# Kernel tuning notes

Hardware: AMD Instinct MI355X
Metric: run time of the kernel (lower is better)

## Reference

```python
import jax, jax.numpy as jnp
import numpy as np

FT = 0.2  # clip floor (init arg ft)

def _norm_mat(m):
    # matrix / (count of nonzeros along last dim + 1e-30)
    deg = jnp.sum(m != 0, axis=-1, keepdims=True).astype(m.dtype)
    return m / (deg + 1e-30)

def _l2n(x):
    return x / (jnp.linalg.norm(x, axis=-1, keepdims=True) + 1e-30)

def setup_inputs():
    B, L, D, H, O = 2, 2048, 64, 64, 128
    N = 2 * L
    ks = jax.random.split(jax.random.key(0), 30)
    u = lambda i, s: jax.random.uniform(ks[i], s, jnp.float32)
    g = lambda i, s: jax.random.normal(ks[i], s, jnp.float32) * 0.05
    inp = {}
    inp['word_outputs_0'] = g(0, (B, L, D))
    inp['word_outputs_1'] = g(1, (B, L, D))
    inp['node_hidden'] = g(2, (B, D))
    inp['op_embedding'] = g(3, (B, O, D))
    inp['word_exist_sequence'] = (u(4, (B, N)) < 0.8).astype(jnp.float32)
    inp['word_exist_matrix'] = (u(5, (B, N, N)) < 0.8).astype(jnp.float32)
    inp['word_operator'] = (u(6, (B, N, O)) < 0.02).astype(jnp.float32)
    inp['word_word'] = (u(7, (B, N, N)) < 0.01).astype(jnp.float32)
    inp['depend_0'] = (u(8, (B, L, L)) < 0.05).astype(jnp.float32)
    inp['depend_1'] = (u(9, (B, L, L)) < 0.05).astype(jnp.float32)
    inp['goal_word'] = u(10, (B, N))
    names = [('Wg', (D, H)), ('bg', (H,)), ('Wwk', (D, H)), ('bwk', (H,)),
             ('Wws', (D, H)), ('bws', (H,)), ('Wo', (D, D)), ('bo', (D,)),
             ('Wupd', (3 * H, D)), ('bupd', (D,)), ('Wf', (3 * H + D, D)), ('bf', (D,)),
             ('Wf2', (2 * D, D)), ('bf2', (D,)), ('Wout', (D, D)), ('bout', (D,))]
    for i, (nm, s) in enumerate(names):
        inp[nm] = g(11 + i, s)
    return inp

def _forward(w0, w1, nh, opE, wes, wem, wop, ww, d0, d1, gw,
             Wg, bg, Wwk, bwk, Wws, bws, Wo, bo, Wupd, bupd, Wf, bf, Wf2, bf2, Wout, bout):
    all_w = jnp.concatenate([w0, w1], axis=1)                      # [B,N,D]
    goal_trans = (nh @ Wg + bg)[:, None, :]                        # [B,1,H] (broadcast = expand)
    word_g = _l2n(goal_trans * gw[..., None])                      # [B,N,H]
    word_w_k = _l2n(jnp.matmul(_norm_mat(ww * wem), all_w @ Wwk + bwk))
    ws0 = jnp.matmul(_norm_mat(d0), w0 @ Wws + bws)
    ws1 = jnp.matmul(_norm_mat(d1), w1 @ Wws + bws)
    word_w_s = _l2n(jnp.concatenate([ws0, ws1], axis=1))           # [B,N,H]
    neigh = jnp.concatenate([word_g, word_w_k, word_w_s], axis=-1)  # [B,N,3H]
    forget = jax.nn.sigmoid(jnp.concatenate([all_w, word_g, word_w_k, word_w_s], axis=-1) @ Wf + bf)
    word_updated = jnp.maximum(forget, FT) * all_w + (1.0 - forget) * jax.nn.relu(neigh @ Wupd + bupd)
    adj_op = _norm_mat(jnp.swapaxes(wes[..., None] * wop, 1, 2))   # [B,O,N]
    word_op = jnp.matmul(adj_op, word_updated @ Wo + bo)           # [B,O,D]
    forget2 = jax.nn.sigmoid(jnp.concatenate([opE, word_op], axis=-1) @ Wf2 + bf2)
    op_out = jnp.maximum(forget2, FT) * opE + (1.0 - forget2) * jax.nn.relu(word_op @ Wout + bout)
    # original returns (split(word_updated), op_embedding); concat along node axis here
    return jnp.concatenate([word_updated, op_out], axis=1)         # [B,N+O,D]

def reference(word_outputs_0, word_outputs_1, node_hidden, op_embedding,
              word_exist_sequence, word_exist_matrix, word_operator, word_word,
              depend_0, depend_1, goal_word,
              Wg, bg, Wwk, bwk, Wws, bws, Wo, bo, Wupd, bupd, Wf, bf, Wf2, bf2, Wout, bout):
    return _forward(word_outputs_0, word_outputs_1, node_hidden, op_embedding,
                    word_exist_sequence, word_exist_matrix, word_operator, word_word,
                    depend_0, depend_1, goal_word,
                    Wg, bg, Wwk, bwk, Wws, bws, Wo, bo, Wupd, bupd, Wf, bf, Wf2, bf2, Wout, bout)
```

## Files before the change

kernel.cpp:

```cpp
#include <hip/hip_runtime.h>
#include <cstdint>

typedef unsigned short u16;
typedef unsigned long long u64;

__device__ __forceinline__ u16 f2b(float f){
  union { float f; uint32_t i; } v; v.f = f;
  uint32_t r = v.i + 0x7FFFu + ((v.i >> 16) & 1u);
  return (u16)(r >> 16);
}
__device__ __forceinline__ float b2f(u16 u){
  union { uint32_t i; float f; } v; v.i = ((uint32_t)u) << 16; return v.f;
}
__device__ __forceinline__ float sigmoidf(float x){ return 1.0f / (1.0f + __expf(-x)); }

__global__ void k_pre(const float* __restrict__ nh, const float* __restrict__ Wg,
                      const float* __restrict__ bg, float* __restrict__ ghat){
  int b = threadIdx.x >> 6, h = threadIdx.x & 63;
  float g = bg[h];
  for (int d = 0; d < 64; ++d) g += nh[b*64 + d] * Wg[d*64 + h];
  float ss = g * g;
  #pragma unroll
  for (int o = 32; o > 0; o >>= 1) ss += __shfl_xor(ss, o, 64);
  ghat[b*64 + h] = g / (sqrtf(ss) + 1e-30f);
}

__global__ __launch_bounds__(256) void k_xform(
    const float* __restrict__ w0, const float* __restrict__ w1,
    const float* __restrict__ Wwk, const float* __restrict__ bwk,
    const float* __restrict__ Wws, const float* __restrict__ bws,
    float* __restrict__ Xk, float* __restrict__ Xs){
  __shared__ float sWk[4096], sWs[4096];
  int tid = threadIdx.x;
  for (int i = tid; i < 1024; i += 256){
    ((float4*)sWk)[i] = ((const float4*)Wwk)[i];
    ((float4*)sWs)[i] = ((const float4*)Wws)[i];
  }
  __syncthreads();
  int lane = tid & 63, wave = tid >> 6;
  float bk = bwk[lane], bs = bws[lane];
  float aw[4];
  #pragma unroll
  for (int t = 0; t < 4; ++t){
    int row = blockIdx.x*4 + wave + t*2048;
    int b = row >> 12, n = row & 4095;
    aw[t] = (n < 2048) ? w0[((size_t)(b*2048 + n))*64 + lane]
                       : w1[((size_t)(b*2048 + n - 2048))*64 + lane];
  }
  #pragma unroll
  for (int t = 0; t < 4; ++t){
    int row = blockIdx.x*4 + wave + t*2048;
    float xk = bk, xs = bs;
    #pragma unroll 8
    for (int d = 0; d < 64; ++d){
      float a = __shfl(aw[t], d, 64);
      xk += a * sWk[d*64 + lane];
      xs += a * sWs[d*64 + lane];
    }
    Xk[(size_t)row*64 + lane] = xk;
    Xs[(size_t)row*64 + lane] = xs;
  }
}

__global__ __launch_bounds__(256) void k_bits_all(
    const float* __restrict__ ww, const float* __restrict__ wem,
    const float* __restrict__ d0, const float* __restrict__ d1,
    u64* __restrict__ bitBig, u64* __restrict__ bitD0, u64* __restrict__ bitD1){
  int wid = blockIdx.x*4 + (threadIdx.x >> 6);
  int lane = threadIdx.x & 63;
  const float *A, *B; u64* dst;
  if (wid < 32768){
    A = ww + (size_t)wid*1024; B = wem + (size_t)wid*1024; dst = bitBig + (size_t)wid*16;
  } else if (wid < 40960){
    size_t c = wid - 32768; A = d0 + c*1024; B = A; dst = bitD0 + c*16;
  } else {
    size_t c = wid - 40960; A = d1 + c*1024; B = A; dst = bitD1 + c*16;
  }
  const float4* ap = (const float4*)A + lane;
  const float4* bp = (const float4*)B + lane;
  float4 a0 = ap[0], a1 = ap[64], a2 = ap[128], a3 = ap[192];
  float4 b0 = bp[0], b1 = bp[64], b2 = bp[128], b3 = bp[192];
  u64 myw = 0;
#define B4(i, va, vb) { \
  u64 m0 = __ballot((va.x != 0.f) && (vb.x != 0.f)); \
  u64 m1 = __ballot((va.y != 0.f) && (vb.y != 0.f)); \
  u64 m2 = __ballot((va.z != 0.f) && (vb.z != 0.f)); \
  u64 m3 = __ballot((va.w != 0.f) && (vb.w != 0.f)); \
  if (lane == (i)*4 + 0) myw = m0; \
  if (lane == (i)*4 + 1) myw = m1; \
  if (lane == (i)*4 + 2) myw = m2; \
  if (lane == (i)*4 + 3) myw = m3; }
  B4(0, a0, b0) B4(1, a1, b1) B4(2, a2, b2) B4(3, a3, b3)
#undef B4
  if (lane < 16) dst[lane] = myw;
}

__global__ __launch_bounds__(64) void k_bitsop(
    const float* __restrict__ wes, const float* __restrict__ wop, u64* __restrict__ bitOp){
  int lane = threadIdx.x;
  int ng = blockIdx.x;
  float2 v = ((const float2*)(wop + (size_t)ng*128))[lane];
  float e = wes[ng];
  u64 m0 = __ballot((e != 0.f) && (v.x != 0.f));
  u64 m1 = __ballot((e != 0.f) && (v.y != 0.f));
  if (lane == 0) bitOp[(size_t)ng*2]     = m0;
  if (lane == 1) bitOp[(size_t)ng*2 + 1] = m1;
}

__global__ __launch_bounds__(256) void k_gath_all(
    const u64* __restrict__ bitBig, const u64* __restrict__ bitD0, const u64* __restrict__ bitD1,
    const float* __restrict__ Xk, const float* __restrict__ Xs,
    u16* __restrict__ wwkn, u16* __restrict__ wwsn){
  __shared__ int q[4][256];
  int lane = threadIdx.x & 63, wave = threadIdx.x >> 6;
  int wid = blockIdx.x*4 + wave;
  const u64* bits; const float* Xb; u16* op; int WPR;
  if (wid < 8192){
    WPR = 64; bits = bitBig + (size_t)wid*64;
    int b = wid >> 12;
    Xb = Xk + (size_t)b*4096*64 + lane;
    op = wwkn + (size_t)wid*64;
  } else if (wid < 12288){
    int lr = wid - 8192; WPR = 32; bits = bitD0 + (size_t)lr*32;
    int b = lr >> 11, r = lr & 2047;
    Xb = Xs + (size_t)b*4096*64 + lane;
    op = wwsn + ((size_t)b*4096 + r)*64;
  } else {
    int lr = wid - 12288; WPR = 32; bits = bitD1 + (size_t)lr*32;
    int b = lr >> 11, r = lr & 2047;
    Xb = Xs + ((size_t)b*4096 + 2048)*64 + lane;
    op = wwsn + ((size_t)b*4096 + 2048 + r)*64;
  }
  u64 word = (lane < WPR) ? bits[lane] : 0ULL;
  int c = __popcll(word);
  int pre = c;
  #pragma unroll
  for (int off = 1; off < 64; off <<= 1){
    int t = __shfl_up(pre, off, 64);
    if (lane >= off) pre += t;
  }
  int total = __shfl(pre, 63, 64);
  int base = pre - c;
  int colhi = (lane >> 2) * 256 + (lane & 3);
  u64 m = word;
  while (m){
    int p = __builtin_ctzll(m); m &= m - 1;
    q[wave][base++] = colhi + p*4;
  }
  __syncthreads();
  float acc = 0.f;
  int i = 0;
  for (; i + 8 <= total; i += 8){
    int4 c0 = *(const int4*)&q[wave][i];
    int4 c1 = *(const int4*)&q[wave][i + 4];
    float v0 = Xb[(size_t)c0.x*64], v1 = Xb[(size_t)c0.y*64];
    float v2 = Xb[(size_t)c0.z*64], v3 = Xb[(size_t)c0.w*64];
    float v4 = Xb[(size_t)c1.x*64], v5 = Xb[(size_t)c1.y*64];
    float v6 = Xb[(size_t)c1.z*64], v7 = Xb[(size_t)c1.w*64];
    acc += ((v0 + v1) + (v2 + v3)) + ((v4 + v5) + (v6 + v7));
  }
  for (; i < total; ++i) acc += Xb[(size_t)q[wave][i]*64];
  float ss = acc * acc;
  #pragma unroll
  for (int o = 32; o > 0; o >>= 1) ss += __shfl_xor(ss, o, 64);
  op[lane] = f2b(acc / (sqrtf(ss) + 1e-30f));
}

__global__ __launch_bounds__(256, 2) void k_update(
    const float* __restrict__ w0, const float* __restrict__ w1,
    const float* __restrict__ gw, const float* __restrict__ ghat,
    const u16* __restrict__ wwkn, const u16* __restrict__ wwsn,
    const float* __restrict__ Wf, const float* __restrict__ bf,
    const float* __restrict__ Wupd, const float* __restrict__ bupd,
    const float* __restrict__ Wo, const float* __restrict__ bo,
    float* __restrict__ out, float* __restrict__ WUo){
  __shared__ uint32_t pWf[8192];
  __shared__ uint32_t pWu[6144];
  __shared__ uint32_t pWo[2048];
  __shared__ float xsh[4][256];
  int tid = threadIdx.x;
  for (int i = tid; i < 8192; i += 256){
    int k2 = i >> 6, ln = i & 63;
    pWf[i] = (uint32_t)f2b(Wf[(2*k2)*64 + ln]) | ((uint32_t)f2b(Wf[(2*k2+1)*64 + ln]) << 16);
  }
  for (int i = tid; i < 6144; i += 256){
    int k2 = i >> 6, ln = i & 63;
    pWu[i] = (uint32_t)f2b(Wupd[(2*k2)*64 + ln]) | ((uint32_t)f2b(Wupd[(2*k2+1)*64 + ln]) << 16);
  }
  for (int i = tid; i < 2048; i += 256){
    int k2 = i >> 6, ln = i & 63;
    pWo[i] = (uint32_t)f2b(Wo[(2*k2)*64 + ln]) | ((uint32_t)f2b(Wo[(2*k2+1)*64 + ln]) << 16);
  }
  __syncthreads();
  int lane = tid & 63, wave = tid >> 6;
  float bff = bf[lane], bup = bupd[lane], boo = bo[lane];
  float aw[4], wgv[4], wk[4], wsv[4];
  #pragma unroll
  for (int t = 0; t < 4; ++t){
    int row = blockIdx.x*4 + wave + t*2048;
    int b = row >> 12, n = row & 4095;
    aw[t] = (n < 2048) ? w0[((size_t)(b*2048 + n))*64 + lane]
                       : w1[((size_t)(b*2048 + n - 2048))*64 + lane];
    float gvv = gw[b*4096 + n];
    wgv[t] = (gvv != 0.f) ? ghat[b*64 + lane] : 0.f;
    wk[t]  = b2f(wwkn[(size_t)row*64 + lane]);
    wsv[t] = b2f(wwsn[(size_t)row*64 + lane]);
  }
  #pragma unroll
  for (int t = 0; t < 4; ++t){
    int row = blockIdx.x*4 + wave + t*2048;
    int b = row >> 12, n = row & 4095;
    xsh[wave][lane] = aw[t]; xsh[wave][64 + lane] = wgv[t];
    xsh[wave][128 + lane] = wk[t]; xsh[wave][192 + lane] = wsv[t];
    float f = bff, u = bup;
    #pragma unroll 8
    for (int k2 = 0; k2 < 32; ++k2){
      float2 xv = *(const float2*)&xsh[wave][2*k2];
      uint32_t wf = pWf[k2*64 + lane];
      f += xv.x * b2f((u16)wf) + xv.y * b2f((u16)(wf >> 16));
    }
    #pragma unroll 8
    for (int k2 = 32; k2 < 128; ++k2){
      float2 xv = *(const float2*)&xsh[wave][2*k2];
      uint32_t wf = pWf[k2*64 + lane];
      uint32_t wu = pWu[(k2 - 32)*64 + lane];
      f += xv.x * b2f((u16)wf) + xv.y * b2f((u16)(wf >> 16));
      u += xv.x * b2f((u16)wu) + xv.y * b2f((u16)(wu >> 16));
    }
    f = sigmoidf(f);
    u = fmaxf(u, 0.f);
    float wu = fmaxf(f, 0.2f) * aw[t] + (1.f - f) * u;
    out[((size_t)b*4224 + n)*64 + lane] = wu;
    float o = boo;
    #pragma unroll 8
    for (int k2 = 0; k2 < 32; ++k2){
      uint32_t wo2 = pWo[k2*64 + lane];
      o += __shfl(wu, 2*k2, 64) * b2f((u16)wo2) + __shfl(wu, 2*k2 + 1, 64) * b2f((u16)(wo2 >> 16));
    }
    WUo[(size_t)row*64 + lane] = o;
  }
}

__global__ __launch_bounds__(256) void k_opagg(
    const u64* __restrict__ bitOp, const float* __restrict__ WUo,
    float* __restrict__ wordop){
  __shared__ int q[4][96];
  __shared__ float sacc[4][64];
  __shared__ int scnt[4];
  int tid = threadIdx.x, lane = tid & 63, wave = tid >> 6;
  int rowIdx = blockIdx.x;
  int b = rowIdx >> 7, o = rowIdx & 127;
  int wrd = o & 1, bit = o >> 1;
  const u64* bp = bitOp + (size_t)b*8192 + (size_t)wave*2048 + wrd;
  u64 lt = (1ULL << lane) - 1ULL;
  u64 vv[16];
  #pragma unroll
  for (int it = 0; it < 16; ++it) vv[it] = bp[(size_t)(it*64 + lane)*2];
  int cnt = 0;
  #pragma unroll
  for (int it = 0; it < 16; ++it){
    bool nz = (vv[it] >> bit) & 1ULL;
    u64 m = __ballot(nz);
    if (nz) q[wave][cnt + (int)__popcll(m & lt)] = wave*1024 + it*64 + lane;
    cnt += (int)__popcll(m);
  }
  const float* Xb = WUo + (size_t)b*4096*64 + lane;
  float acc = 0.f;
  int i = 0;
  for (; i + 8 <= cnt; i += 8){
    int4 c0 = *(const int4*)&q[wave][i];
    int4 c1 = *(const int4*)&q[wave][i + 4];
    float v0 = Xb[(size_t)c0.x*64], v1 = Xb[(size_t)c0.y*64];
    float v2 = Xb[(size_t)c0.z*64], v3 = Xb[(size_t)c0.w*64];
    float v4 = Xb[(size_t)c1.x*64], v5 = Xb[(size_t)c1.y*64];
    float v6 = Xb[(size_t)c1.z*64], v7 = Xb[(size_t)c1.w*64];
    acc += ((v0 + v1) + (v2 + v3)) + ((v4 + v5) + (v6 + v7));
  }
  for (; i < cnt; ++i) acc += Xb[(size_t)q[wave][i]*64];
  sacc[wave][lane] = acc;
  if (lane == 0) scnt[wave] = cnt;
  __syncthreads();
  if (wave == 0){
    float t = sacc[0][lane] + sacc[1][lane] + sacc[2][lane] + sacc[3][lane];
    float deg = (float)(scnt[0] + scnt[1] + scnt[2] + scnt[3]);
    wordop[(size_t)rowIdx*64 + lane] = t / (deg + 1e-30f);
  }
}

__global__ __launch_bounds__(256) void k_opout(
    const float* __restrict__ opE, const float* __restrict__ wordop,
    const float* __restrict__ Wf2, const float* __restrict__ bf2,
    const float* __restrict__ Wout, const float* __restrict__ bout,
    float* __restrict__ out){
  __shared__ float sW2[8192];
  __shared__ float sWo[4096];
  __shared__ float xsh[4][128];
  int tid = threadIdx.x;
  for (int i = tid; i < 2048; i += 256) ((float4*)sW2)[i] = ((const float4*)Wf2)[i];
  for (int i = tid; i < 1024; i += 256) ((float4*)sWo)[i] = ((const float4*)Wout)[i];
  __syncthreads();
  int lane = tid & 63, wave = tid >> 6;
  int row = blockIdx.x*4 + wave;
  int b = row >> 7, o = row & 127;
  float e  = opE[(size_t)row*64 + lane];
  float wo = wordop[(size_t)row*64 + lane];
  xsh[wave][lane] = e; xsh[wave][64 + lane] = wo;
  float f = bf2[lane], u = bout[lane];
  #pragma unroll 8
  for (int k = 0; k < 128; ++k) f += xsh[wave][k] * sW2[k*64 + lane];
  #pragma unroll 8
  for (int d = 0; d < 64; ++d)  u += xsh[wave][64 + d] * sWo[d*64 + lane];
  f = sigmoidf(f);
  u = fmaxf(u, 0.f);
  float res = fmaxf(f, 0.2f) * e + (1.f - f) * u;
  out[((size_t)b*4224 + 4096 + o)*64 + lane] = res;
}

extern "C" void kernel_launch(void* const* d_in, const int* in_sizes, int n_in,
                              void* d_out, int out_size, void* d_ws, size_t ws_size,
                              hipStream_t stream){
  const float* w0   = (const float*)d_in[0];
  const float* w1   = (const float*)d_in[1];
  const float* nh   = (const float*)d_in[2];
  const float* opE  = (const float*)d_in[3];
  const float* wes  = (const float*)d_in[4];
  const float* wem  = (const float*)d_in[5];
  const float* wop  = (const float*)d_in[6];
  const float* ww   = (const float*)d_in[7];
  const float* d0   = (const float*)d_in[8];
  const float* d1   = (const float*)d_in[9];
  const float* gw   = (const float*)d_in[10];
  const float* Wg   = (const float*)d_in[11];
  const float* bg   = (const float*)d_in[12];
  const float* Wwk  = (const float*)d_in[13];
  const float* bwk  = (const float*)d_in[14];
  const float* Wws  = (const float*)d_in[15];
  const float* bws  = (const float*)d_in[16];
  const float* Wo   = (const float*)d_in[17];
  const float* bo   = (const float*)d_in[18];
  const float* Wupd = (const float*)d_in[19];
  const float* bupd = (const float*)d_in[20];
  const float* Wf   = (const float*)d_in[21];
  const float* bf   = (const float*)d_in[22];
  const float* Wf2  = (const float*)d_in[23];
  const float* bf2  = (const float*)d_in[24];
  const float* Wout = (const float*)d_in[25];
  const float* bout = (const float*)d_in[26];

  float* ws   = (float*)d_ws;
  float* ghat = ws;
  float* Xk   = ws + 128;
  float* Xs   = ws + 524416;
  float* wopm = ws + 1048704;
  u64*  bitBig= (u64*)(ws + 1065088);
  u64*  bitD0 = (u64*)(ws + 2113664);
  u64*  bitD1 = (u64*)(ws + 2375808);
  u64*  bitOp = (u64*)(ws + 2637952);
  u16*  wwkn  = (u16*)(ws + 2670720);
  u16*  wwsn  = (u16*)(ws + 2932864);
  float* WUo  = Xs;
  float* out  = (float*)d_out;

  k_pre<<<1, 128, 0, stream>>>(nh, Wg, bg, ghat);
  k_xform<<<512, 256, 0, stream>>>(w0, w1, Wwk, bwk, Wws, bws, Xk, Xs);
  k_bits_all<<<12288, 256, 0, stream>>>(ww, wem, d0, d1, bitBig, bitD0, bitD1);
  k_bitsop<<<8192, 64, 0, stream>>>(wes, wop, bitOp);
  k_gath_all<<<4096, 256, 0, stream>>>(bitBig, bitD0, bitD1, Xk, Xs, wwkn, wwsn);
  k_update<<<512, 256, 0, stream>>>(w0, w1, gw, ghat, wwkn, wwsn, Wf, bf, Wupd, bupd, Wo, bo, out, WUo);
  k_opagg<<<256, 256, 0, stream>>>(bitOp, WUo, wopm);
  k_opout<<<64, 256, 0, stream>>>(opE, wopm, Wf2, bf2, Wout, bout, out);
}
```

Before: 456.7 us.

## Stage bitmask and gather loads through direct global-to-LDS loads

Switches k_bits_all to load its float rows straight into LDS with global_load_lds before the ballot, and switches k_gath_all's neighbour-row gather to batches of 16 direct-to-LDS loads followed by LDS reads. It also removes the __syncthreads after the per-wave queue build. The aim is more memory-level parallelism and fewer VGPR round trips on the bandwidth-bound bit extraction and sparse gather. The cost is extra LDS traffic and a waitcnt-based sync, and correctness depends on the global-to-LDS builtin's lane/offset semantics and on waitcnt also covering the LDS writes.

```diff
diff --git a/kernel.cpp b/kernel.cpp
--- a/kernel.cpp
+++ b/kernel.cpp
@@ -13,6 +13,16 @@
   union { uint32_t i; float f; } v; v.i = ((uint32_t)u) << 16; return v.f;
 }
 __device__ __forceinline__ float sigmoidf(float x){ return 1.0f / (1.0f + __expf(-x)); }
+
+__device__ __forceinline__ void gl_lds16(const void* g, void* l){
+  __builtin_amdgcn_global_load_lds((const __attribute__((address_space(1))) void*)g,
+                                   (__attribute__((address_space(3))) void*)l, 16, 0, 0);
+}
+__device__ __forceinline__ void gl_lds4(const void* g, void* l){
+  __builtin_amdgcn_global_load_lds((const __attribute__((address_space(1))) void*)g,
+                                   (__attribute__((address_space(3))) void*)l, 4, 0, 0);
+}
+#define WAIT_VM0() __builtin_amdgcn_s_waitcnt(0x0F70)
 
 __global__ void k_pre(const float* __restrict__ nh, const float* __restrict__ Wg,
                       const float* __restrict__ bg, float* __restrict__ ghat){
@@ -66,20 +76,33 @@
     const float* __restrict__ ww, const float* __restrict__ wem,
     const float* __restrict__ d0, const float* __restrict__ d1,
     u64* __restrict__ bitBig, u64* __restrict__ bitD0, u64* __restrict__ bitD1){
-  int wid = blockIdx.x*4 + (threadIdx.x >> 6);
-  int lane = threadIdx.x & 63;
-  const float *A, *B; u64* dst;
+  __shared__ float lA[4][1024];
+  __shared__ float lB[4][1024];
+  int wave = threadIdx.x >> 6, lane = threadIdx.x & 63;
+  int wid = blockIdx.x*4 + wave;
+  const float *A, *B; u64* dst; bool two;
   if (wid < 32768){
-    A = ww + (size_t)wid*1024; B = wem + (size_t)wid*1024; dst = bitBig + (size_t)wid*16;
+    A = ww + (size_t)wid*1024; B = wem + (size_t)wid*1024;
+    dst = bitBig + (size_t)wid*16; two = true;
   } else if (wid < 40960){
-    size_t c = wid - 32768; A = d0 + c*1024; B = A; dst = bitD0 + c*16;
+    size_t c = wid - 32768; A = d0 + c*1024; B = A; dst = bitD0 + c*16; two = false;
   } else {
-    size_t c = wid - 40960; A = d1 + c*1024; B = A; dst = bitD1 + c*16;
-  }
-  const float4* ap = (const float4*)A + lane;
-  const float4* bp = (const float4*)B + lane;
-  float4 a0 = ap[0], a1 = ap[64], a2 = ap[128], a3 = ap[192];
-  float4 b0 = bp[0], b1 = bp[64], b2 = bp[128], b3 = bp[192];
+    size_t c = wid - 40960; A = d1 + c*1024; B = A; dst = bitD1 + c*16; two = false;
+  }
+  #pragma unroll
+  for (int i = 0; i < 4; ++i)
+    gl_lds16(A + i*256 + lane*4, &lA[wave][i*256]);
+  if (two){
+    #pragma unroll
+    for (int i = 0; i < 4; ++i)
+      gl_lds16(B + i*256 + lane*4, &lB[wave][i*256]);
+  }
+  WAIT_VM0();
+  const float4* a4 = (const float4*)lA[wave];
+  const float4* b4 = (const float4*)lB[wave];
+  float4 a0 = a4[lane], a1 = a4[64 + lane], a2 = a4[128 + lane], a3 = a4[192 + lane];
+  float4 b0 = two ? b4[lane] : a0, b1 = two ? b4[64 + lane] : a1;
+  float4 b2 = two ? b4[128 + lane] : a2, b3 = two ? b4[192 + lane] : a3;
   u64 myw = 0;
 #define B4(i, va, vb) { \
   u64 m0 = __ballot((va.x != 0.f) && (vb.x != 0.f)); \
@@ -112,23 +135,24 @@
     const float* __restrict__ Xk, const float* __restrict__ Xs,
     u16* __restrict__ wwkn, u16* __restrict__ wwsn){
   __shared__ int q[4][256];
+  __shared__ float rows[4][16][64];
   int lane = threadIdx.x & 63, wave = threadIdx.x >> 6;
   int wid = blockIdx.x*4 + wave;
-  const u64* bits; const float* Xb; u16* op; int WPR;
+  const u64* bits; const float* XbBase; u16* op; int WPR;
   if (wid < 8192){
     WPR = 64; bits = bitBig + (size_t)wid*64;
     int b = wid >> 12;
-    Xb = Xk + (size_t)b*4096*64 + lane;
+    XbBase = Xk + (size_t)b*4096*64;
     op = wwkn + (size_t)wid*64;
   } else if (wid < 12288){
     int lr = wid - 8192; WPR = 32; bits = bitD0 + (size_t)lr*32;
     int b = lr >> 11, r = lr & 2047;
-    Xb = Xs + (size_t)b*4096*64 + lane;
+    XbBase = Xs + (size_t)b*4096*64;
     op = wwsn + ((size_t)b*4096 + r)*64;
   } else {
     int lr = wid - 12288; WPR = 32; bits = bitD1 + (size_t)lr*32;
     int b = lr >> 11, r = lr & 2047;
-    Xb = Xs + ((size_t)b*4096 + 2048)*64 + lane;
+    XbBase = Xs + ((size_t)b*4096 + 2048)*64;
     op = wwsn + ((size_t)b*4096 + 2048 + r)*64;
   }
   u64 word = (lane < WPR) ? bits[lane] : 0ULL;
@@ -147,19 +171,41 @@
     int p = __builtin_ctzll(m); m &= m - 1;
     q[wave][base++] = colhi + p*4;
   }
-  __syncthreads();
   float acc = 0.f;
   int i = 0;
-  for (; i + 8 <= total; i += 8){
+  for (; i + 16 <= total; i += 16){
     int4 c0 = *(const int4*)&q[wave][i];
     int4 c1 = *(const int4*)&q[wave][i + 4];
-    float v0 = Xb[(size_t)c0.x*64], v1 = Xb[(size_t)c0.y*64];
-    float v2 = Xb[(size_t)c0.z*64], v3 = Xb[(size_t)c0.w*64];
-    float v4 = Xb[(size_t)c1.x*64], v5 = Xb[(size_t)c1.y*64];
-    float v6 = Xb[(size_t)c1.z*64], v7 = Xb[(size_t)c1.w*64];
-    acc += ((v0 + v1) + (v2 + v3)) + ((v4 + v5) + (v6 + v7));
-  }
-  for (; i < total; ++i) acc += Xb[(size_t)q[wave][i]*64];
+    int4 c2 = *(const int4*)&q[wave][i + 8];
+    int4 c3 = *(const int4*)&q[wave][i + 12];
+    gl_lds4(XbBase + (size_t)c0.x*64 + lane, &rows[wave][ 0][0]);
+    gl_lds4(XbBase + (size_t)c0.y*64 + lane, &rows[wave][ 1][0]);
+    gl_lds4(XbBase + (size_t)c0.z*64 + lane, &rows[wave][ 2][0]);
+    gl_lds4(XbBase + (size_t)c0.w*64 + lane, &rows[wave][ 3][0]);
+    gl_lds4(XbBase + (size_t)c1.x*64 + lane, &rows[wave][ 4][0]);
+    gl_lds4(XbBase + (size_t)c1.y*64 + lane, &rows[wave][ 5][0]);
+    gl_lds4(XbBase + (size_t)c1.z*64 + lane, &rows[wave][ 6][0]);
+    gl_lds4(XbBase + (size_t)c1.w*64 + lane, &rows[wave][ 7][0]);
+    gl_lds4(XbBase + (size_t)c2.x*64 + lane, &rows[wave][ 8][0]);
+    gl_lds4(XbBase + (size_t)c2.y*64 + lane, &rows[wave][ 9][0]);
+    gl_lds4(XbBase + (size_t)c2.z*64 + lane, &rows[wave][10][0]);
+    gl_lds4(XbBase + (size_t)c2.w*64 + lane, &rows[wave][11][0]);
+    gl_lds4(XbBase + (size_t)c3.x*64 + lane, &rows[wave][12][0]);
+    gl_lds4(XbBase + (size_t)c3.y*64 + lane, &rows[wave][13][0]);
+    gl_lds4(XbBase + (size_t)c3.z*64 + lane, &rows[wave][14][0]);
+    gl_lds4(XbBase + (size_t)c3.w*64 + lane, &rows[wave][15][0]);
+    WAIT_VM0();
+    float s0 = 0.f, s1 = 0.f, s2 = 0.f, s3 = 0.f;
+    #pragma unroll
+    for (int r = 0; r < 4; ++r){
+      s0 += rows[wave][r][lane];
+      s1 += rows[wave][4 + r][lane];
+      s2 += rows[wave][8 + r][lane];
+      s3 += rows[wave][12 + r][lane];
+    }
+    acc += (s0 + s1) + (s2 + s3);
+  }
+  for (; i < total; ++i) acc += XbBase[(size_t)q[wave][i]*64 + lane];
   float ss = acc * acc;
   #pragma unroll
   for (int o = 32; o > 0; o >>= 1) ss += __shfl_xor(ss, o, 64);
```

New measurement: 463.6 us. Within noise of the previous version (+1.5%).
